# Kernel optimization log

Hardware: AMD Instinct MI355X
Metric: run time of the kernel (lower is better)

The kernel has to match this reference:

```python
import jax, jax.numpy as jnp
import numpy as np

KH = KW = 3
PAD = 1
OFFG = 8  # offset groups: 144 offset channels / (2*9)


def conv2d(x, w, b, pad=PAD):
    out = jax.lax.conv_general_dilated(
        x, w, window_strides=(1, 1), padding=[(pad, pad), (pad, pad)],
        dimension_numbers=('NCHW', 'OIHW', 'NCHW'))
    return out + b[None, :, None, None]


def deform_conv2d(x, offset, w, b):
    # x: [B,C,H,W], offset: [B, 2*K*OFFG, H, W] (per group: (y,x) per kernel tap)
    B, C, H, W = x.shape
    K = KH * KW
    Cg = C // OFFG
    off = offset.reshape(B, OFFG, K, 2, H, W)
    ky, kx = jnp.meshgrid(jnp.arange(KH), jnp.arange(KW), indexing='ij')
    ky = ky.reshape(K).astype(x.dtype)
    kx = kx.reshape(K).astype(x.dtype)
    ys = (jnp.arange(H) - PAD).astype(x.dtype)  # stride 1, dilation 1
    xs = (jnp.arange(W) - PAD).astype(x.dtype)
    # sampling positions [B, OFFG, K, H, W]
    py = ys[None, None, None, :, None] + ky[None, None, :, None, None] + off[:, :, :, 0]
    px = xs[None, None, None, None, :] + kx[None, None, :, None, None] + off[:, :, :, 1]
    y0 = jnp.floor(py)
    x0 = jnp.floor(px)
    xg = x.reshape(B, OFFG, Cg, H * W)
    cols = jnp.zeros((B, OFFG, Cg, K, H, W), x.dtype)
    for dy in (0, 1):
        for dx in (0, 1):
            yi = y0 + dy
            xi = x0 + dx
            wgt = (1.0 - jnp.abs(py - yi)) * (1.0 - jnp.abs(px - xi))
            valid = (yi >= 0) & (yi < H) & (xi >= 0) & (xi < W)
            yc = jnp.clip(yi, 0, H - 1).astype(jnp.int32)
            xc = jnp.clip(xi, 0, W - 1).astype(jnp.int32)
            idx = (yc * W + xc).reshape(B, OFFG, 1, K * H * W)
            g = jnp.take_along_axis(xg, idx, axis=3).reshape(B, OFFG, Cg, K, H, W)
            cols = cols + g * (wgt * valid.astype(x.dtype))[:, :, None]
    cols = cols.reshape(B, C, K, H, W)
    out = jnp.einsum('bckhw,ock->bohw', cols, w.reshape(w.shape[0], C, K))
    return out + b[None, :, None, None]


def setup_inputs() -> dict:
    key = jax.random.key(0)
    ks = jax.random.split(key, 6)
    B, C, H, W = 16, 144, 64, 64
    feat_arm = jax.random.normal(ks[0], (B, C, H, W), jnp.float32)
    feat_up = jax.random.normal(ks[1], (B, C, H, W), jnp.float32)
    # offset conv: in=288 (cat), out=144 = 2*9*OFFG; small init so offsets are sane
    off_w = jax.random.normal(ks[2], (144, 288, 3, 3), jnp.float32) * 0.01
    off_b = jnp.zeros((144,), jnp.float32)
    dcn_w = jax.random.normal(ks[3], (256, 144, 3, 3), jnp.float32) * (1.0 / np.sqrt(144 * 9))
    dcn_b = jnp.zeros((256,), jnp.float32)
    return {'feat_arm': feat_arm, 'feat_up': feat_up, 'off_w': off_w,
            'off_b': off_b, 'dcn_w': dcn_w, 'dcn_b': dcn_b}


def reference(feat_arm, feat_up, off_w, off_b, dcn_w, dcn_b):
    x = jnp.concatenate([feat_arm, feat_up], axis=1)  # [B, 288, H, W]
    offset = conv2d(x, off_w, off_b)                  # [B, 144, H, W]
    y = deform_conv2d(feat_up, offset, dcn_w, dcn_b)  # [B, 256, H, W]
    return jax.nn.silu(y)
```

## Files before the change

### kernel.cpp

```cpp
#include <hip/hip_runtime.h>
#include <math.h>

constexpr int BN = 16;
constexpr int C_IN = 144, C_CAT = 288, C_OFF = 144, C_OUT = 256;
constexpr int OFFG = 8, CG = 18;

constexpr int FUB_ELEMS  = C_IN * BN * 4096;
constexpr int OFFP_ELEMS = BN * 72 * 4096;
constexpr int WOFF_PACK = 9 * 9 * 9 * 512;
constexpr int WDCN_PACK = 8 * 6 * 16 * 512;

typedef __attribute__((ext_vector_type(8))) short bf16x8;
typedef __attribute__((ext_vector_type(8))) _Float16 f16x8;
typedef __attribute__((ext_vector_type(2))) _Float16 f16x2;
typedef __attribute__((ext_vector_type(4))) float f32x4;
typedef __attribute__((ext_vector_type(4))) unsigned u32x4;

__device__ __forceinline__ unsigned short f2bf(float f) {
  unsigned u = __builtin_bit_cast(unsigned, f);
  return (unsigned short)((u + 0x7FFFu + ((u >> 16) & 1u)) >> 16);
}

__device__ __forceinline__ unsigned packh2(float a, float b) {
  unsigned short ha = __builtin_bit_cast(unsigned short, (_Float16)a);
  unsigned short hb = __builtin_bit_cast(unsigned short, (_Float16)b);
  return (unsigned)ha | ((unsigned)hb << 16);
}
__device__ __forceinline__ float h2f_lo(unsigned u) {
  return (float)__builtin_bit_cast(_Float16, (unsigned short)(u & 0xFFFFu));
}
__device__ __forceinline__ float h2f_hi(unsigned u) {
  return (float)__builtin_bit_cast(_Float16, (unsigned short)(u >> 16));
}

__device__ __forceinline__ void gload_lds16(const void* g, void* l) {
  __builtin_amdgcn_global_load_lds(
      (const __attribute__((address_space(1))) unsigned*)g,
      (__attribute__((address_space(3))) unsigned*)l, 16, 0, 0);
}

__global__ __launch_bounds__(256) void prep(
    const float* __restrict__ fu, _Float16* __restrict__ fuB,
    const float* __restrict__ off_w, const float* __restrict__ dcn_w,
    unsigned short* __restrict__ wo, _Float16* __restrict__ wd) {
  int idx = blockIdx.x * 256 + threadIdx.x;
  int i4 = idx * 4;
  if (i4 < FUB_ELEMS) {
    float4 v = *(const float4*)(fu + i4);
    f16x2 a = {(_Float16)v.x, (_Float16)v.y};
    f16x2 b = {(_Float16)v.z, (_Float16)v.w};
    *(unsigned*)(fuB + i4) = __builtin_bit_cast(unsigned, a);
    *(unsigned*)(fuB + i4 + 2) = __builtin_bit_cast(unsigned, b);
  }
  if (idx < WOFF_PACK) {
    int i = idx & 7, lane = (idx >> 3) & 63, t = idx >> 9;
    int mt = t % 9; t /= 9;
    int tap = t % 9, cb = t / 9;
    int co = mt * 16 + (lane & 15);
    int ci = cb * 32 + ((lane >> 4) << 3) + i;
    wo[idx] = f2bf(off_w[(co * C_CAT + ci) * 9 + tap]);
  }
  if (idx < WDCN_PACK) {
    int i = idx & 7, lane = (idx >> 3) & 63, t = idx >> 9;
    int mt = t & 15; t >>= 4;
    int ks = t % 6, g = t / 6;
    int co = mt * 16 + (lane & 15);
    int r = ks * 32 + ((lane >> 4) << 3) + i;
    float v = 0.f;
    if (r < 162) {
      int ci = r / 9, tap = r - ci * 9;
      v = dcn_w[(co * C_IN + g * CG + ci) * 9 + tap];
    }
    wd[idx] = (_Float16)v;
  }
}

__global__ __launch_bounds__(256) void offs_conv_mfma(
    const float* __restrict__ fa, const float* __restrict__ fu,
    const unsigned short* __restrict__ wt, const float* __restrict__ bias,
    unsigned* __restrict__ offp) {
  const int bid = (blockIdx.x & 7) * 64 + (blockIdx.x >> 3);
  const int b = bid >> 5;
  const int y0 = (bid & 31) << 1;
  const int tid = threadIdx.x;
  const int wave = tid >> 6, lane = tid & 63;
  const int kg = lane >> 4, ln = lane & 15;

  __shared__ __align__(16) unsigned short xs[4 * 66 * 32];

  f32x4 acc[9][2];
#pragma unroll
  for (int m = 0; m < 9; ++m)
#pragma unroll
    for (int n = 0; n < 2; ++n) acc[m][n] = {0.f, 0.f, 0.f, 0.f};

  for (int cb = 0; cb < 9; ++cb) {
    __syncthreads();
    for (int idx = tid; idx < 2112; idx += 256) {
      int q = idx / 264;
      int rem = idx - q * 264;
      int row = rem / 66;
      int cc = rem - row * 66;
      int y = y0 - 1 + row, x = cc - 1;
      ushort4 wv = make_ushort4(0, 0, 0, 0);
      if (y >= 0 && y < 64 && x >= 0 && x < 64) {
        int cib = cb * 32 + (q << 2);
        const float* p = (cib < C_IN)
                             ? fa + (((size_t)(b * C_IN + cib)) << 12)
                             : fu + (((size_t)(b * C_IN + cib - C_IN)) << 12);
        int o = (y << 6) + x;
        wv.x = f2bf(p[o]);
        wv.y = f2bf(p[o + 4096]);
        wv.z = f2bf(p[o + 8192]);
        wv.w = f2bf(p[o + 12288]);
      }
      int e = ((row * 66 + cc) << 5) + (((q >> 1) ^ (cc & 3)) << 3) + ((q & 1) << 2);
      *(ushort4*)&xs[e] = wv;
    }
    __syncthreads();

    for (int tap = 0; tap < 9; ++tap) {
      const int ky = tap / 3, kx = tap - ky * 3;
      bf16x8 a[9];
      const unsigned short* wp = wt + (((size_t)(cb * 9 + tap) * 9) << 9) + (lane << 3);
#pragma unroll
      for (int m = 0; m < 9; ++m) a[m] = *(const bf16x8*)(wp + (m << 9));
#pragma unroll
      for (int n = 0; n < 2; ++n) {
        int px = ((wave << 1) + n) * 16 + ln;
        int row = (px >> 6) + ky, cc = (px & 63) + kx;
        int e = ((row * 66 + cc) << 5) + ((kg ^ (cc & 3)) << 3);
        bf16x8 bv = *(const bf16x8*)&xs[e];
        __builtin_amdgcn_s_setprio(1);
#pragma unroll
        for (int m = 0; m < 9; ++m)
          acc[m][n] = __builtin_amdgcn_mfma_f32_16x16x32_bf16(a[m], bv, acc[m][n], 0, 0, 0);
        __builtin_amdgcn_s_setprio(0);
      }
    }
  }

#pragma unroll
  for (int n = 0; n < 2; ++n) {
    int px = ((wave << 1) + n) * 16 + ln;
    int y = y0 + (px >> 6), x = px & 63;
#pragma unroll
    for (int m = 0; m < 9; ++m) {
      int cob = m * 16 + (kg << 2);
#pragma unroll
      for (int rr = 0; rr < 4; rr += 2) {
        unsigned v = packh2(acc[m][n][rr] + bias[cob + rr],
                            acc[m][n][rr + 1] + bias[cob + rr + 1]);
        offp[(((size_t)(b * 72 + ((cob + rr) >> 1))) << 12) + (y << 6) + x] = v;
      }
    }
  }
}

__global__ __launch_bounds__(512, 4) void dcn_mfma(
    const _Float16* __restrict__ fuB, const unsigned* __restrict__ offp,
    const _Float16* __restrict__ wt, const float* __restrict__ bias,
    float* __restrict__ out) {
  const int bid = (blockIdx.x & 7) * 128 + (blockIdx.x >> 3);
  const int b = bid >> 6, h = bid & 63;
  const int tid = threadIdx.x;
  const int wave = tid >> 6, lane = tid & 63;
  const int kg = lane >> 4, ln = lane & 15;
  const int wm = wave >> 2, wn = wave & 3;
  const int px = (wn << 4) + ln;

  __shared__ __align__(16) unsigned short colsT[64 * 202];
  __shared__ __align__(16) _Float16 wl[3][8192];

  f32x4 acc[8];
#pragma unroll
  for (int m = 0; m < 8; ++m) acc[m] = {0.f, 0.f, 0.f, 0.f};

  for (int i = tid; i < 64 * 15; i += 512) {
    int p = i / 15, d = i - p * 15;
    *(unsigned*)&colsT[p * 202 + 162 + 2 * d] = 0u;
  }

  {
    const _Float16* src = wt + (wave * 2) * 512 + lane * 8;
#pragma unroll
    for (int j = 0; j < 2; ++j)
      gload_lds16(src + j * 512, &wl[0][(wave * 2 + j) * 512]);
  }

  auto make_geo = [&](int gg_, int tap, int p) -> uint4 {
    int ky = tap / 3, kx = tap - ky * 3;
    unsigned op = offp[(((size_t)(b * 72 + gg_ * 9 + tap)) << 12) + (h << 6) + p];
    float oy = h2f_lo(op), ox = h2f_hi(op);
    float py = (float)(h - 1 + ky) + oy;
    float pxs = (float)(p - 1 + kx) + ox;
    float y0f = floorf(py), x0f = floorf(pxs);
    int y0 = (int)y0f, x0 = (int)x0f;
    float fy = py - y0f, fx = pxs - x0f;
    float vy0 = (y0 >= 0 && y0 < 64) ? 1.f : 0.f;
    float vy1 = (y0 + 1 >= 0 && y0 + 1 < 64) ? 1.f : 0.f;
    float vx0 = (x0 >= 0 && x0 < 64) ? 1.f : 0.f;
    float vx1 = (x0 + 1 >= 0 && x0 + 1 < 64) ? 1.f : 0.f;
    float a0 = (1.f - fx) * vx0;
    float a1 = fx * vx1;
    float wlo = (x0 == -1) ? a1 : (x0 == 63 ? 0.f : a0);
    float whi = (x0 == 63) ? a0 : (x0 == -1 ? 0.f : a1);
    int xL = min(max(x0, 0), 62);
    int yc0 = min(max(y0, 0), 63), yc1 = min(max(y0 + 1, 0), 63);
    float cy0 = (1.f - fy) * vy0, cy1 = fy * vy1;
    uint4 r;
    r.x = (unsigned)((yc0 << 6) + xL) | ((unsigned)((yc1 << 6) + xL) << 16);
    r.y = 0u;
    r.z = packh2(cy0 * wlo, cy0 * whi);
    r.w = packh2(cy1 * wlo, cy1 * whi);
    return r;
  };

  int tg = 0, cur = 0;
  for (int g = 0; g < OFFG; ++g) {
    __syncthreads();

    uint4 gg = make_geo(g, wave, lane);
    uint4 g8 = make_geo(g, 8, lane);

    const _Float16* gbase = fuB + (((size_t)(b * C_IN + g * CG)) << 12);
    {
      const int iL0 = gg.x & 0xFFFFu, iL1 = gg.x >> 16;
      const f16x2 w0 = __builtin_bit_cast(f16x2, gg.z);
      const f16x2 w1 = __builtin_bit_cast(f16x2, gg.w);
      const int j0 = g8.x & 0xFFFFu, j1 = g8.x >> 16;
      const f16x2 u0 = __builtin_bit_cast(f16x2, g8.z);
      const f16x2 u1 = __builtin_bit_cast(f16x2, g8.w);
      const int n8 = (wave < 2) ? 3 : 2;

      unsigned d0[18], d1[18], e0[3], e1[3];
#pragma unroll
      for (int u = 0; u < 18; ++u) {
        const _Float16* pl = gbase + ((size_t)u << 12);
        __builtin_memcpy(&d0[u], pl + iL0, 4);
        __builtin_memcpy(&d1[u], pl + iL1, 4);
      }
#pragma unroll
      for (int u = 0; u < 3; ++u) {
        if (u < n8) {
          const _Float16* pl = gbase + ((size_t)(wave + 8 * u) << 12);
          __builtin_memcpy(&e0[u], pl + j0, 4);
          __builtin_memcpy(&e1[u], pl + j1, 4);
        }
      }
#pragma unroll
      for (int u = 0; u < 18; ++u) {
        f16x2 sp = __builtin_bit_cast(f16x2, d0[u]) * w0 +
                   __builtin_bit_cast(f16x2, d1[u]) * w1;
        _Float16 s = sp[0] + sp[1];
        colsT[lane * 202 + u * 9 + wave] = __builtin_bit_cast(unsigned short, s);
      }
#pragma unroll
      for (int u = 0; u < 3; ++u) {
        if (u < n8) {
          f16x2 sp = __builtin_bit_cast(f16x2, e0[u]) * u0 +
                     __builtin_bit_cast(f16x2, e1[u]) * u1;
          _Float16 s = sp[0] + sp[1];
          colsT[lane * 202 + (wave + 8 * u) * 9 + 8] =
              __builtin_bit_cast(unsigned short, s);
        }
      }
    }
    __syncthreads();

    for (int ks = 0; ks < 6; ++ks, ++tg) {
      int cbase = px * 202 + ks * 32 + (kg << 3);
      u32x4 bu;
      bu[0] = *(const unsigned*)&colsT[cbase];
      bu[1] = *(const unsigned*)&colsT[cbase + 2];
      bu[2] = *(const unsigned*)&colsT[cbase + 4];
      bu[3] = *(const unsigned*)&colsT[cbase + 6];
      f16x8 bv = __builtin_bit_cast(f16x8, bu);

      int nxt = cur + 1;
      if (nxt == 3) nxt = 0;
      if (tg < 47) {
        const _Float16* src =
            wt + (size_t)(tg + 1) * 8192 + (wave * 2) * 512 + lane * 8;
        _Float16* dst = wl[nxt];
#pragma unroll
        for (int j = 0; j < 2; ++j)
          gload_lds16(src + j * 512, dst + (wave * 2 + j) * 512);
        asm volatile("s_waitcnt vmcnt(2)" ::: "memory");
      } else {
        asm volatile("s_waitcnt vmcnt(0)" ::: "memory");
      }
      __builtin_amdgcn_s_barrier();

      const _Float16* wbuf = wl[cur] + (wm * 8) * 512 + lane * 8;
      __builtin_amdgcn_s_setprio(1);
#pragma unroll
      for (int j = 0; j < 8; ++j) {
        f16x8 av = *(const f16x8*)(wbuf + j * 512);
        acc[j] = __builtin_amdgcn_mfma_f32_16x16x32_f16(av, bv, acc[j], 0, 0, 0);
      }
      __builtin_amdgcn_s_setprio(0);
      cur = nxt;
    }
  }

#pragma unroll
  for (int j = 0; j < 8; ++j) {
    int cob = (wm * 8 + j) * 16 + (kg << 2);
#pragma unroll
    for (int r = 0; r < 4; ++r) {
      float y = acc[j][r] + bias[cob + r];
      out[(((size_t)(b * C_OUT + cob + r)) << 12) + (h << 6) + px] =
          y / (1.f + expf(-y));
    }
  }
}

extern "C" void kernel_launch(void* const* d_in, const int* in_sizes, int n_in,
                              void* d_out, int out_size, void* d_ws, size_t ws_size,
                              hipStream_t stream) {
  const float* feat_arm = (const float*)d_in[0];
  const float* feat_up  = (const float*)d_in[1];
  const float* off_w    = (const float*)d_in[2];
  const float* off_b    = (const float*)d_in[3];
  const float* dcn_w    = (const float*)d_in[4];
  const float* dcn_b    = (const float*)d_in[5];
  float* out = (float*)d_out;

  _Float16* fuB = (_Float16*)d_ws;
  unsigned* offp = (unsigned*)(fuB + FUB_ELEMS);
  unsigned short* wo = (unsigned short*)(offp + OFFP_ELEMS);
  _Float16* wd = (_Float16*)(wo + WOFF_PACK);

  prep<<<FUB_ELEMS / 1024, 256, 0, stream>>>(feat_up, fuB, off_w, dcn_w, wo, wd);
  offs_conv_mfma<<<BN * 32, 256, 0, stream>>>(feat_arm, feat_up, wo, off_b, offp);
  dcn_mfma<<<BN * 64, 512, 0, stream>>>(fuB, offp, wd, dcn_b, out);
}
```

Measured before the change: 249.5 us.

## Fuse fp16 feature conversion into offset conv and prefetch next-group gathers

The separate prep pass that converted feat_up to fp16 is removed. The offset-conv kernel now writes the fp16 copy as a side effect of the loads it already does, using only the interior rows of each tile so every pixel is written once. In the deformable conv kernel, the bilinear gather loads and geometry for the next offset group are issued early, during the previous group's MFMA loop, with a relaxed vmcnt wait so their latency overlaps compute. The cost is higher register pressure from keeping the prefetched values live across the loop, and the offset conv now has extra global stores.

```diff
diff --git a/kernel.cpp b/kernel.cpp
--- a/kernel.cpp
+++ b/kernel.cpp
@@ -40,18 +40,9 @@
 }
 
 __global__ __launch_bounds__(256) void prep(
-    const float* __restrict__ fu, _Float16* __restrict__ fuB,
     const float* __restrict__ off_w, const float* __restrict__ dcn_w,
     unsigned short* __restrict__ wo, _Float16* __restrict__ wd) {
   int idx = blockIdx.x * 256 + threadIdx.x;
-  int i4 = idx * 4;
-  if (i4 < FUB_ELEMS) {
-    float4 v = *(const float4*)(fu + i4);
-    f16x2 a = {(_Float16)v.x, (_Float16)v.y};
-    f16x2 b = {(_Float16)v.z, (_Float16)v.w};
-    *(unsigned*)(fuB + i4) = __builtin_bit_cast(unsigned, a);
-    *(unsigned*)(fuB + i4 + 2) = __builtin_bit_cast(unsigned, b);
-  }
   if (idx < WOFF_PACK) {
     int i = idx & 7, lane = (idx >> 3) & 63, t = idx >> 9;
     int mt = t % 9; t /= 9;
@@ -78,7 +69,7 @@
 __global__ __launch_bounds__(256) void offs_conv_mfma(
     const float* __restrict__ fa, const float* __restrict__ fu,
     const unsigned short* __restrict__ wt, const float* __restrict__ bias,
-    unsigned* __restrict__ offp) {
+    unsigned* __restrict__ offp, _Float16* __restrict__ fuB) {
   const int bid = (blockIdx.x & 7) * 64 + (blockIdx.x >> 3);
   const int b = bid >> 5;
   const int y0 = (bid & 31) << 1;
@@ -109,10 +100,18 @@
                              ? fa + (((size_t)(b * C_IN + cib)) << 12)
                              : fu + (((size_t)(b * C_IN + cib - C_IN)) << 12);
         int o = (y << 6) + x;
-        wv.x = f2bf(p[o]);
-        wv.y = f2bf(p[o + 4096]);
-        wv.z = f2bf(p[o + 8192]);
-        wv.w = f2bf(p[o + 12288]);
+        float v0 = p[o], v1 = p[o + 4096], v2 = p[o + 8192], v3 = p[o + 12288];
+        wv.x = f2bf(v0);
+        wv.y = f2bf(v1);
+        wv.z = f2bf(v2);
+        wv.w = f2bf(v3);
+        if (cib >= C_IN && row >= 1 && row <= 2) {
+          _Float16* fb = fuB + (((size_t)(b * C_IN + cib - C_IN)) << 12) + o;
+          fb[0] = (_Float16)v0;
+          fb[4096] = (_Float16)v1;
+          fb[8192] = (_Float16)v2;
+          fb[12288] = (_Float16)v3;
+        }
       }
       int e = ((row * 66 + cc) << 5) + (((q >> 1) ^ (cc & 3)) << 3) + ((q & 1) << 2);
       *(ushort4*)&xs[e] = wv;
@@ -168,6 +167,7 @@
   const int kg = lane >> 4, ln = lane & 15;
   const int wm = wave >> 2, wn = wave & 3;
   const int px = (wn << 4) + ln;
+  const int n8 = (wave < 2) ? 3 : 2;
 
   __shared__ __align__(16) unsigned short colsT[64 * 202];
   __shared__ __align__(16) _Float16 wl[3][8192];
@@ -216,38 +216,40 @@
     return r;
   };
 
+  unsigned d0[18], d1[18], e0[3], e1[3];
+  unsigned wz_cur, ww_cur, uz_cur, uw_cur;
+
+  {
+    uint4 g0 = make_geo(0, wave, lane);
+    uint4 g80 = make_geo(0, 8, lane);
+    wz_cur = g0.z; ww_cur = g0.w; uz_cur = g80.z; uw_cur = g80.w;
+    const _Float16* gb = fuB + ((size_t)(b * C_IN) << 12);
+    const int iL0 = g0.x & 0xFFFFu, iL1 = g0.x >> 16;
+    const int j0 = g80.x & 0xFFFFu, j1 = g80.x >> 16;
+#pragma unroll
+    for (int u = 0; u < 18; ++u) {
+      const _Float16* pl = gb + ((size_t)u << 12);
+      __builtin_memcpy(&d0[u], pl + iL0, 4);
+      __builtin_memcpy(&d1[u], pl + iL1, 4);
+    }
+#pragma unroll
+    for (int u = 0; u < 3; ++u) {
+      int ci8 = min(wave + 8 * u, CG - 1);
+      const _Float16* pl = gb + ((size_t)ci8 << 12);
+      __builtin_memcpy(&e0[u], pl + j0, 4);
+      __builtin_memcpy(&e1[u], pl + j1, 4);
+    }
+  }
+
   int tg = 0, cur = 0;
   for (int g = 0; g < OFFG; ++g) {
     __syncthreads();
 
-    uint4 gg = make_geo(g, wave, lane);
-    uint4 g8 = make_geo(g, 8, lane);
-
-    const _Float16* gbase = fuB + (((size_t)(b * C_IN + g * CG)) << 12);
     {
-      const int iL0 = gg.x & 0xFFFFu, iL1 = gg.x >> 16;
-      const f16x2 w0 = __builtin_bit_cast(f16x2, gg.z);
-      const f16x2 w1 = __builtin_bit_cast(f16x2, gg.w);
-      const int j0 = g8.x & 0xFFFFu, j1 = g8.x >> 16;
-      const f16x2 u0 = __builtin_bit_cast(f16x2, g8.z);
-      const f16x2 u1 = __builtin_bit_cast(f16x2, g8.w);
-      const int n8 = (wave < 2) ? 3 : 2;
-
-      unsigned d0[18], d1[18], e0[3], e1[3];
-#pragma unroll
-      for (int u = 0; u < 18; ++u) {
-        const _Float16* pl = gbase + ((size_t)u << 12);
-        __builtin_memcpy(&d0[u], pl + iL0, 4);
-        __builtin_memcpy(&d1[u], pl + iL1, 4);
-      }
-#pragma unroll
-      for (int u = 0; u < 3; ++u) {
-        if (u < n8) {
-          const _Float16* pl = gbase + ((size_t)(wave + 8 * u) << 12);
-          __builtin_memcpy(&e0[u], pl + j0, 4);
-          __builtin_memcpy(&e1[u], pl + j1, 4);
-        }
-      }
+      const f16x2 w0 = __builtin_bit_cast(f16x2, wz_cur);
+      const f16x2 w1 = __builtin_bit_cast(f16x2, ww_cur);
+      const f16x2 u0 = __builtin_bit_cast(f16x2, uz_cur);
+      const f16x2 u1 = __builtin_bit_cast(f16x2, uw_cur);
 #pragma unroll
       for (int u = 0; u < 18; ++u) {
         f16x2 sp = __builtin_bit_cast(f16x2, d0[u]) * w0 +
@@ -286,7 +288,11 @@
 #pragma unroll
         for (int j = 0; j < 2; ++j)
           gload_lds16(src + j * 512, dst + (wave * 2 + j) * 512);
-        asm volatile("s_waitcnt vmcnt(2)" ::: "memory");
+        if (ks == 1 && g < 7) {
+          asm volatile("s_waitcnt vmcnt(44)" ::: "memory");
+        } else {
+          asm volatile("s_waitcnt vmcnt(2)" ::: "memory");
+        }
       } else {
         asm volatile("s_waitcnt vmcnt(0)" ::: "memory");
       }
@@ -301,6 +307,28 @@
       }
       __builtin_amdgcn_s_setprio(0);
       cur = nxt;
+
+      if (ks == 0 && g < 7) {
+        uint4 gn = make_geo(g + 1, wave, lane);
+        uint4 g8n = make_geo(g + 1, 8, lane);
+        wz_cur = gn.z; ww_cur = gn.w; uz_cur = g8n.z; uw_cur = g8n.w;
+        const _Float16* gbn = fuB + (((size_t)(b * C_IN + (g + 1) * CG)) << 12);
+        const int iL0 = gn.x & 0xFFFFu, iL1 = gn.x >> 16;
+        const int j0 = g8n.x & 0xFFFFu, j1 = g8n.x >> 16;
+#pragma unroll
+        for (int u = 0; u < 18; ++u) {
+          const _Float16* pl = gbn + ((size_t)u << 12);
+          __builtin_memcpy(&d0[u], pl + iL0, 4);
+          __builtin_memcpy(&d1[u], pl + iL1, 4);
+        }
+#pragma unroll
+        for (int u = 0; u < 3; ++u) {
+          int ci8 = min(wave + 8 * u, CG - 1);
+          const _Float16* pl = gbn + ((size_t)ci8 << 12);
+          __builtin_memcpy(&e0[u], pl + j0, 4);
+          __builtin_memcpy(&e1[u], pl + j1, 4);
+        }
+      }
     }
   }
 
@@ -332,7 +360,7 @@
   unsigned short* wo = (unsigned short*)(offp + OFFP_ELEMS);
   _Float16* wd = (_Float16*)(wo + WOFF_PACK);
 
-  prep<<<FUB_ELEMS / 1024, 256, 0, stream>>>(feat_up, fuB, off_w, dcn_w, wo, wd);
-  offs_conv_mfma<<<BN * 32, 256, 0, stream>>>(feat_arm, feat_up, wo, off_b, offp);
+  prep<<<(WDCN_PACK + 255) / 256, 256, 0, stream>>>(off_w, dcn_w, wo, wd);
+  offs_conv_mfma<<<BN * 32, 256, 0, stream>>>(feat_arm, feat_up, wo, off_b, offp, fuB);
   dcn_mfma<<<BN * 64, 512, 0, stream>>>(fuB, offp, wd, dcn_b, out);
 }
```

New measurement: 263.7 us. +5.7%, slower.
